# Kernel tuning notes

Measured on AMD Instinct MI355X. Metric: run time of the kernel, lower is better.

## Reference

```python
import jax, jax.numpy as jnp
import numpy as np

D_MODEL = 1024
NUM_HEADS = 16
D_K = D_MODEL // NUM_HEADS  # 64
THETA = 10000.0
B, S = 2, 2048


def _rope(x, cos, sin):
    # x: [b, h, s, d]; cos/sin: [s, d//2] (broadcast over b, h)
    x1 = x[..., 0::2]
    x2 = x[..., 1::2]
    y1 = x1 * cos - x2 * sin
    y2 = x1 * sin + x2 * cos
    # interleave back: stack on last dim then flatten pairs
    return jnp.stack([y1, y2], axis=-1).reshape(x.shape)


def setup_inputs() -> dict:
    key = jax.random.key(0)
    ks = jax.random.split(key, 5)
    scale = 1.0 / np.sqrt(D_MODEL)
    return {
        "x": jax.random.normal(ks[0], (B, S, D_MODEL), dtype=jnp.float32),
        "token_positions": jnp.arange(S, dtype=jnp.int32),
        "Wq": jax.random.normal(ks[1], (D_MODEL, D_MODEL), dtype=jnp.float32) * scale,
        "Wk": jax.random.normal(ks[2], (D_MODEL, D_MODEL), dtype=jnp.float32) * scale,
        "Wv": jax.random.normal(ks[3], (D_MODEL, D_MODEL), dtype=jnp.float32) * scale,
        "Wo": jax.random.normal(ks[4], (D_MODEL, D_MODEL), dtype=jnp.float32) * scale,
    }


def reference(x, token_positions, Wq, Wk, Wv, Wo):
    b, s, _ = x.shape
    # torch nn.Linear semantics (no bias in this repo's Linear): y = x @ W.T
    q = jnp.einsum("bsd,od->bso", x, Wq)
    k = jnp.einsum("bsd,od->bso", x, Wk)
    v = jnp.einsum("bsd,od->bso", x, Wv)
    # split heads: b s (h d) -> b h s d
    def split(t):
        return t.reshape(b, s, NUM_HEADS, D_K).transpose(0, 2, 1, 3)
    q, k, v = split(q), split(k), split(v)

    # RoPE tables
    inv_freq = 1.0 / (THETA ** (jnp.arange(0, D_K, 2, dtype=jnp.float32) / D_K))  # [d/2]
    freqs = token_positions.astype(jnp.float32)[:, None] * inv_freq[None, :]      # [s, d/2]
    cos, sin = jnp.cos(freqs), jnp.sin(freqs)
    q = _rope(q, cos, sin)
    k = _rope(k, cos, sin)

    scale = D_K ** (-0.5)
    scores = jnp.einsum("bhqd,bhkd->bhqk", q, k) * scale  # [b,h,s,s]
    causal = jnp.tril(jnp.ones((s, s), dtype=bool))
    scores = jnp.where(causal, scores, -jnp.inf)
    attn = jax.nn.softmax(scores, axis=-1)
    out = jnp.einsum("bhqk,bhkd->bhqd", attn, v)
    out = out.transpose(0, 2, 1, 3).reshape(b, s, D_MODEL)  # b h s d -> b s (h d)
    return jnp.einsum("bsd,od->bso", out, Wo)
```

## Files before the change

kernel.cpp:

```cpp
#include <hip/hip_runtime.h>
#include <hip/hip_bf16.h>
#include <math.h>

#define SS 2048

typedef __attribute__((ext_vector_type(8))) __bf16 bf16x8;
typedef __attribute__((ext_vector_type(4))) float f32x4;
typedef __attribute__((ext_vector_type(16))) float f32x16;
typedef __attribute__((ext_vector_type(4))) unsigned int u32x4;
typedef __attribute__((ext_vector_type(4))) unsigned short u16x4;

__device__ __forceinline__ f32x4 mfma16(bf16x8 a, bf16x8 b, f32x4 c) {
  return __builtin_amdgcn_mfma_f32_16x16x32_bf16(a, b, c, 0, 0, 0);
}
__device__ __forceinline__ f32x16 mfma32(bf16x8 a, bf16x8 b, f32x16 c) {
  return __builtin_amdgcn_mfma_f32_32x32x16_bf16(a, b, c, 0, 0, 0);
}

__device__ __forceinline__ void gld_lds16(const void* g, void* l) {
  __builtin_amdgcn_global_load_lds(
      (__attribute__((address_space(1))) void*)(g),
      (__attribute__((address_space(3))) void*)(l), 16, 0, 0);
}

#if __has_builtin(__builtin_amdgcn_exp2f)
#define EXP2F(x) __builtin_amdgcn_exp2f(x)
#else
#define EXP2F(x) __expf(0.69314718056f * (x))
#endif

__device__ __forceinline__ unsigned int cvtpk_bf16(float lo, float hi) {
  unsigned int r;
  asm("v_cvt_pk_bf16_f32 %0, %1, %2" : "=v"(r) : "v"(lo), "v"(hi));
  return r;
}
__device__ __forceinline__ void swap32(unsigned int& x, unsigned int& y) {
  asm("v_permlane32_swap_b32 %0, %1" : "+v"(x), "+v"(y));
}
__device__ __forceinline__ unsigned short bfu(float v) {
  __bf16 h = (__bf16)v;
  return __builtin_bit_cast(unsigned short, h);
}

__global__ void prep_kernel(const float* __restrict__ x, const float* __restrict__ Wq,
                            const float* __restrict__ Wk, const float* __restrict__ Wv,
                            const float* __restrict__ Wo, const int* __restrict__ pos,
                            __bf16* __restrict__ xb, __bf16* __restrict__ Wb,
                            float2* __restrict__ tab) {
  const int bid = blockIdx.x, tid = threadIdx.x;
  if (bid >= 4096) {
    int i = (bid - 4096) * 256 + tid;
    int s = i >> 5, j = i & 31;
    float p = (float)pos[s];
    float inv = exp2f((float)j * -0.41524101186098283f);
    float f = p * inv;
    float sn, cs;
    sincosf(f, &sn, &cs);
    tab[i] = make_float2(cs, sn);
    return;
  }
  const float* s;
  __bf16* d;
  size_t base;
  if (bid < 2048) { s = x; d = xb; base = bid; }
  else {
    int seg = (bid - 2048) >> 9;
    s = (seg == 0) ? Wq : (seg == 1) ? Wk : (seg == 2) ? Wv : Wo;
    d = Wb + (size_t)seg * 1024 * 1024;
    base = (bid - 2048) & 511;
  }
  size_t i = (base * 256 + tid) * 8;
  float4 a = *reinterpret_cast<const float4*>(s + i);
  float4 b = *reinterpret_cast<const float4*>(s + i + 4);
  bf16x8 o;
  o[0] = (__bf16)a.x; o[1] = (__bf16)a.y; o[2] = (__bf16)a.z; o[3] = (__bf16)a.w;
  o[4] = (__bf16)b.x; o[5] = (__bf16)b.y; o[6] = (__bf16)b.z; o[7] = (__bf16)b.w;
  *reinterpret_cast<bf16x8*>(d + i) = o;
}

__global__ __launch_bounds__(512, 1) void gemm256_kernel(
    const __bf16* __restrict__ A, const __bf16* __restrict__ Bw,
    __bf16* __restrict__ C, __bf16* __restrict__ Vt,
    const float2* __restrict__ tab) {
  const int K = 1024, N = 3072, nk = 32;
  __shared__ __align__(16) __bf16 sm[57344];
  __bf16* lsA = sm;
  __bf16* lsB = sm + 32768;

  const int tid = threadIdx.x;
  const int lane = tid & 63;
  const int wave = tid >> 6;
  const int wr = wave >> 2, wc = wave & 3;
  const bool lowW = wave < 6;

  const int xcd = blockIdx.x & 7;
  const int ii = blockIdx.x >> 3;
  const int m0 = (2 * xcd + (ii & 1)) * 256;
  const int n0 = (ii >> 1) * 192;

  const f32x4 fzero = {0.f, 0.f, 0.f, 0.f};
  f32x4 acc[8][3];
#pragma unroll
  for (int f = 0; f < 8; ++f)
#pragma unroll
    for (int g = 0; g < 3; ++g) acc[f][g] = fzero;

  const int arow0 = tid >> 2, ac = tid & 3;
  const __bf16* gA0 = A + (size_t)(m0 + arow0) * K + 8 * (ac ^ ((arow0 >> 1) & 3));
  const __bf16* gA1 = A + (size_t)(m0 + 128 + arow0) * K + 8 * (ac ^ (((arow0 + 128) >> 1) & 3));
  const int bid0 = tid, bid1 = tid + 384;
  const int br0 = bid0 >> 2, br1 = bid1 >> 2;
  const __bf16* gB0 = Bw + (size_t)(n0 + br0) * K + 8 * ((bid0 & 3) ^ ((br0 >> 1) & 3));
  const __bf16* gB1 = Bw + (size_t)(n0 + br1) * K + 8 * ((bid1 & 3) ^ ((br1 >> 1) & 3));

#define STAGE256(kt_)                                                \
  do {                                                               \
    const int kc_ = (kt_) & 3;                                       \
    const int ko_ = (kt_) * 32;                                      \
    gld_lds16(gA0 + ko_, lsA + kc_ * 8192 + tid * 8);                \
    gld_lds16(gA1 + ko_, lsA + kc_ * 8192 + 4096 + tid * 8);         \
    if (lowW) {                                                      \
      gld_lds16(gB0 + ko_, lsB + kc_ * 6144 + tid * 8);              \
      gld_lds16(gB1 + ko_, lsB + kc_ * 6144 + 3072 + tid * 8);       \
    }                                                                \
  } while (0)

  STAGE256(0);
  STAGE256(1);

  const int lrow = lane & 15, hi = lane >> 4;

#pragma unroll 1
  for (int kt = 0; kt < nk; ++kt) {
    const int ksA = (kt & 3) * 8192, ksB = (kt & 3) * 6144;
    if (kt + 2 < nk) {
      STAGE256(kt + 2);
      if (lowW) asm volatile("s_waitcnt vmcnt(8)" ::: "memory");
      else      asm volatile("s_waitcnt vmcnt(4)" ::: "memory");
    } else if (kt == nk - 2) {
      if (lowW) asm volatile("s_waitcnt vmcnt(4)" ::: "memory");
      else      asm volatile("s_waitcnt vmcnt(2)" ::: "memory");
    } else {
      asm volatile("s_waitcnt vmcnt(0)" ::: "memory");
    }
    __builtin_amdgcn_s_barrier();

    bf16x8 bfr[3];
#pragma unroll
    for (int g = 0; g < 3; ++g) {
      const int r = wc * 48 + g * 16 + lrow;
      bfr[g] = *reinterpret_cast<const bf16x8*>(
          lsB + ksB + r * 32 + ((hi ^ ((r >> 1) & 3)) * 8));
    }
    bf16x8 af[4];
#pragma unroll
    for (int f = 0; f < 4; ++f) {
      const int r = wr * 128 + f * 16 + lrow;
      af[f] = *reinterpret_cast<const bf16x8*>(
          lsA + ksA + r * 32 + ((hi ^ ((r >> 1) & 3)) * 8));
    }
    __builtin_amdgcn_s_setprio(1);
#pragma unroll
    for (int f = 0; f < 4; ++f)
#pragma unroll
      for (int g = 0; g < 3; ++g) acc[f][g] = mfma16(af[f], bfr[g], acc[f][g]);
    __builtin_amdgcn_s_setprio(0);
#pragma unroll
    for (int f = 0; f < 4; ++f) {
      const int r = wr * 128 + (f + 4) * 16 + lrow;
      af[f] = *reinterpret_cast<const bf16x8*>(
          lsA + ksA + r * 32 + ((hi ^ ((r >> 1) & 3)) * 8));
    }
    __builtin_amdgcn_s_setprio(1);
#pragma unroll
    for (int f = 0; f < 4; ++f)
#pragma unroll
      for (int g = 0; g < 3; ++g) acc[f + 4][g] = mfma16(af[f], bfr[g], acc[f + 4][g]);
    __builtin_amdgcn_s_setprio(0);
  }
#undef STAGE256

  const int crow = (lane >> 4) * 4, ccol = lane & 15;
  const int par = ccol & 1;
#pragma unroll
  for (int g = 0; g < 3; ++g) {
    const int cb = n0 + wc * 48 + g * 16;
    if (cb < 2048) {
      const int jj = ((cb + ccol) >> 1) & 31;
#pragma unroll
      for (int f = 0; f < 8; ++f) {
#pragma unroll
        for (int t = 0; t < 4; ++t) {
          const int r = m0 + wr * 128 + f * 16 + crow + t;
          const int s = r & (SS - 1);
          float2 cs = tab[(s << 5) | jj];
          float v = acc[f][g][t];
          float o = __shfl_xor(v, 1);
          float y = par ? fmaf(o, cs.y, v * cs.x) : fmaf(v, cs.x, -o * cs.y);
          C[(size_t)r * N + cb + ccol] = (__bf16)y;
        }
      }
    } else {
      const int c = cb - 2048 + ccol;
      const int hh = c >> 6, dd = c & 63;
#pragma unroll
      for (int f = 0; f < 8; ++f) {
        const int r0 = m0 + wr * 128 + f * 16 + crow;
        const int bb = r0 >> 11, s0 = r0 & (SS - 1);
        u16x4 pk;
#pragma unroll
        for (int t = 0; t < 4; ++t) pk[t] = bfu(acc[f][g][t]);
        *reinterpret_cast<u16x4*>(Vt + ((size_t)(bb * 16 + hh) * 64 + dd) * SS + s0) = pk;
      }
    }
  }
}

__global__ __launch_bounds__(512, 1) void gemm_out_kernel(
    const __bf16* __restrict__ A, const __bf16* __restrict__ Bw,
    float* __restrict__ C) {
  const int K = 1024, N = 1024, nk = 32;
  __shared__ __align__(16) __bf16 sm[32768];
  __bf16* lsA = sm;
  __bf16* lsB = sm + 16384;

  const int tid = threadIdx.x;
  const int lane = tid & 63;
  const int wave = tid >> 6;
  const int wr = wave >> 2, wc = wave & 3;

  const int xcd = blockIdx.x & 7;
  const int ii = blockIdx.x >> 3;
  const int m0 = (4 * xcd + (ii & 3)) * 128;
  const int n0 = (ii >> 2) * 128;

  const f32x4 fzero = {0.f, 0.f, 0.f, 0.f};
  f32x4 acc[4][2];
#pragma unroll
  for (int f = 0; f < 4; ++f)
#pragma unroll
    for (int g = 0; g < 2; ++g) acc[f][g] = fzero;

  const int srow = tid >> 2, sc = tid & 3;
  const int ssc = 8 * (sc ^ ((srow >> 1) & 3));
  const __bf16* gA = A + (size_t)(m0 + srow) * K + ssc;
  const __bf16* gB = Bw + (size_t)(n0 + srow) * K + ssc;

#define STAGEO(kt_)                                        \
  do {                                                     \
    const int kc_ = (kt_) & 3;                             \
    gld_lds16(gA + (kt_) * 32, lsA + kc_ * 4096 + tid * 8);\
    gld_lds16(gB + (kt_) * 32, lsB + kc_ * 4096 + tid * 8);\
  } while (0)

  STAGEO(0);
  STAGEO(1);

  const int lrow = lane & 15, hi = lane >> 4;

#pragma unroll 1
  for (int kt = 0; kt < nk; ++kt) {
    const int ks = (kt & 3) * 4096;
    if (kt + 2 < nk) {
      STAGEO(kt + 2);
      asm volatile("s_waitcnt vmcnt(4)" ::: "memory");
    } else if (kt == nk - 2) {
      asm volatile("s_waitcnt vmcnt(2)" ::: "memory");
    } else {
      asm volatile("s_waitcnt vmcnt(0)" ::: "memory");
    }
    __builtin_amdgcn_s_barrier();

    bf16x8 bfr[2], af[4];
#pragma unroll
    for (int g = 0; g < 2; ++g) {
      const int r = wc * 32 + g * 16 + lrow;
      bfr[g] = *reinterpret_cast<const bf16x8*>(
          lsB + ks + r * 32 + ((hi ^ ((r >> 1) & 3)) * 8));
    }
#pragma unroll
    for (int f = 0; f < 4; ++f) {
      const int r = wr * 64 + f * 16 + lrow;
      af[f] = *reinterpret_cast<const bf16x8*>(
          lsA + ks + r * 32 + ((hi ^ ((r >> 1) & 3)) * 8));
    }
    __builtin_amdgcn_s_setprio(1);
#pragma unroll
    for (int f = 0; f < 4; ++f)
#pragma unroll
      for (int g = 0; g < 2; ++g) acc[f][g] = mfma16(af[f], bfr[g], acc[f][g]);
    __builtin_amdgcn_s_setprio(0);
  }
#undef STAGEO

  const int crow = (lane >> 4) * 4, ccol = lane & 15;
#pragma unroll
  for (int f = 0; f < 4; ++f) {
#pragma unroll
    for (int g = 0; g < 2; ++g) {
      int r = m0 + wr * 64 + f * 16 + crow;
      int c = n0 + wc * 32 + g * 16 + ccol;
#pragma unroll
      for (int t = 0; t < 4; ++t) C[(size_t)(r + t) * N + c] = acc[f][g][t];
    }
  }
}

#define CEXP 0.18033688011112042f
#define SHIFT_B 16.0f

#define EXPSUM(S0, S1, L)                                                   \
  {                                                                         \
    float a0_ = 0.f, a1_ = 0.f, a2_ = 0.f, a3_ = 0.f;                       \
    _Pragma("unroll") for (int r = 0; r < 16; r += 4) {                     \
      S0[r] = EXP2F(fmaf(S0[r], CEXP, -SHIFT_B)); a0_ += S0[r];             \
      S0[r + 1] = EXP2F(fmaf(S0[r + 1], CEXP, -SHIFT_B)); a1_ += S0[r + 1]; \
      S0[r + 2] = EXP2F(fmaf(S0[r + 2], CEXP, -SHIFT_B)); a2_ += S0[r + 2]; \
      S0[r + 3] = EXP2F(fmaf(S0[r + 3], CEXP, -SHIFT_B)); a3_ += S0[r + 3]; \
    }                                                                       \
    _Pragma("unroll") for (int r = 0; r < 16; r += 4) {                     \
      S1[r] = EXP2F(fmaf(S1[r], CEXP, -SHIFT_B)); a0_ += S1[r];             \
      S1[r + 1] = EXP2F(fmaf(S1[r + 1], CEXP, -SHIFT_B)); a1_ += S1[r + 1]; \
      S1[r + 2] = EXP2F(fmaf(S1[r + 2], CEXP, -SHIFT_B)); a2_ += S1[r + 2]; \
      S1[r + 3] = EXP2F(fmaf(S1[r + 3], CEXP, -SHIFT_B)); a3_ += S1[r + 3]; \
    }                                                                       \
    float rs_ = (a0_ + a1_) + (a2_ + a3_);                                  \
    rs_ += __shfl_xor(rs_, 32);                                             \
    L += rs_;                                                               \
  }

template <int SPLIT>
__global__ __launch_bounds__(128) void attn_kernel(const __bf16* __restrict__ qkv,
                                                   const __bf16* __restrict__ Vt,
                                                   __bf16* __restrict__ pA,
                                                   __bf16* __restrict__ pB,
                                                   float* __restrict__ pL) {
  const int bid = blockIdx.x;
  const int x = bid & 7, t8 = bid >> 3;
  const int low = t8 & 7, phi = (t8 >> 3) & 3, g = (t8 >> 5) & 3;
  const int half = SPLIT ? (t8 >> 7) : 0;
  const int hp = phi * 8 + x;
  const int b = hp >> 4, h = hp & 15;
  const int qt = (g == 0) ? low : (g == 1) ? 31 - low : (g == 2) ? 15 - low : 16 + low;

  const int nkt = qt + 1;
  const int mid = (nkt + 1) >> 1;
  const int k0 = SPLIT ? (half ? mid : 0) : 0;
  const int k1 = SPLIT ? (half ? nkt : mid) : nkt;

  const int tid = threadIdx.x;
  const int wave = tid >> 6, lane = tid & 63;
  const int q32 = lane & 31, hi = lane >> 5;
  const int qw0 = qt * 64 + wave * 32;
  const int q = qw0 + q32;

  __shared__ __align__(16) __bf16 smem[16384];

  bf16x8 qb[4];
  {
    const __bf16* qr = qkv + (size_t)(b * SS + q) * 3072 + h * 64;
#pragma unroll
    for (int slot = 0; slot < 4; ++slot)
      qb[slot] = *reinterpret_cast<const bf16x8*>(qr + slot * 16 + hi * 8);
  }
  asm volatile("s_waitcnt vmcnt(0)" ::: "memory");

  const __bf16* kbase = qkv + (size_t)(b * SS) * 3072 + 1024 + h * 64;
  const __bf16* vbase = Vt + (size_t)((b * 16 + h) * 64) * SS;

  const int srow = tid >> 3, scg = tid & 7;
  const int ssc = 8 * (scg ^ (srow & 7));
  const __bf16* kG0 = kbase + (size_t)srow * 3072 + ssc;
  const __bf16* vG0 = vbase + (size_t)srow * SS + ssc;

#define STAGE(buf_, kt_)                                                      \
  do {                                                                        \
    const __bf16* kG = kG0 + (size_t)(kt_)*64 * 3072;                         \
    const __bf16* vG = vG0 + (size_t)(kt_)*64;                                \
    __bf16* sl_ = smem + (buf_)*8192;                                         \
    _Pragma("unroll") for (int u = 0; u < 4; ++u) {                           \
      gld_lds16(kG + (size_t)u * 16 * 3072, sl_ + tid * 8 + u * 1024);        \
      gld_lds16(vG + (size_t)u * 16 * SS, sl_ + 4096 + tid * 8 + u * 1024);   \
    }                                                                         \
  } while (0)

  const f32x16 fz16 = {0,0,0,0,0,0,0,0,0,0,0,0,0,0,0,0};
  f32x16 o0 = fz16, o1 = fz16;
  float lsum = 0.f;

  if (k0 < k1) STAGE(0, k0);

#pragma unroll 1
  for (int kt = k0; kt < k1; ++kt) {
    const int buf = (kt - k0) & 1;
    if (kt + 1 < k1) {
      STAGE(buf ^ 1, kt + 1);
      asm volatile("s_waitcnt vmcnt(8)" ::: "memory");
    } else {
      asm volatile("s_waitcnt vmcnt(0)" ::: "memory");
    }
    __builtin_amdgcn_s_barrier();

    const __bf16* lk = smem + buf * 8192;
    const __bf16* lv = lk + 4096;

    f32x16 s0 = fz16, s1 = fz16;
    __builtin_amdgcn_s_setprio(1);
#pragma unroll
    for (int slot = 0; slot < 4; ++slot) {
      const int swz = 8 * ((slot * 2 + hi) ^ (q32 & 7));
      bf16x8 kf0 = *reinterpret_cast<const bf16x8*>(lk + q32 * 64 + swz);
      bf16x8 kf1 = *reinterpret_cast<const bf16x8*>(lk + (32 + q32) * 64 + swz);
      s0 = mfma32(kf0, qb[slot], s0);
      s1 = mfma32(kf1, qb[slot], s1);
    }
    __builtin_amdgcn_s_setprio(0);

    if (kt == qt) {
      const int kvb = kt * 64;
#pragma unroll
      for (int r = 0; r < 16; ++r) {
        const int rowc = (r & 3) + 8 * (r >> 2) + 4 * hi;
        if (kvb + rowc > q) s0[r] = -INFINITY;
        if (kvb + 32 + rowc > q) s1[r] = -INFINITY;
      }
    }

    EXPSUM(s0, s1, lsum)

    bf16x8 pb[4];
    {
      unsigned int A = cvtpk_bf16(s0[0], s0[1]), B2 = cvtpk_bf16(s0[2], s0[3]);
      unsigned int C2 = cvtpk_bf16(s0[4], s0[5]), D2 = cvtpk_bf16(s0[6], s0[7]);
      swap32(A, C2); swap32(B2, D2);
      u32x4 t0 = {A, B2, C2, D2};
      pb[0] = __builtin_bit_cast(bf16x8, t0);
      unsigned int E = cvtpk_bf16(s0[8], s0[9]), F = cvtpk_bf16(s0[10], s0[11]);
      unsigned int G = cvtpk_bf16(s0[12], s0[13]), H = cvtpk_bf16(s0[14], s0[15]);
      swap32(E, G); swap32(F, H);
      u32x4 t1 = {E, F, G, H};
      pb[1] = __builtin_bit_cast(bf16x8, t1);
      unsigned int A3 = cvtpk_bf16(s1[0], s1[1]), B3 = cvtpk_bf16(s1[2], s1[3]);
      unsigned int C3 = cvtpk_bf16(s1[4], s1[5]), D3 = cvtpk_bf16(s1[6], s1[7]);
      swap32(A3, C3); swap32(B3, D3);
      u32x4 t2 = {A3, B3, C3, D3};
      pb[2] = __builtin_bit_cast(bf16x8, t2);
      unsigned int E3 = cvtpk_bf16(s1[8], s1[9]), F3 = cvtpk_bf16(s1[10], s1[11]);
      unsigned int G3 = cvtpk_bf16(s1[12], s1[13]), H3 = cvtpk_bf16(s1[14], s1[15]);
      swap32(E3, G3); swap32(F3, H3);
      u32x4 t3 = {E3, F3, G3, H3};
      pb[3] = __builtin_bit_cast(bf16x8, t3);
    }

    __builtin_amdgcn_s_setprio(1);
#pragma unroll
    for (int slot = 0; slot < 4; ++slot) {
      const int swz = 8 * ((slot * 2 + hi) ^ (q32 & 7));
      bf16x8 v0 = *reinterpret_cast<const bf16x8*>(lv + q32 * 64 + swz);
      bf16x8 v1 = *reinterpret_cast<const bf16x8*>(lv + (32 + q32) * 64 + swz);
      o0 = mfma32(v0, pb[slot], o0);
      o1 = mfma32(v1, pb[slot], o1);
    }
    __builtin_amdgcn_s_setprio(0);

    __builtin_amdgcn_s_barrier();
  }

  asm volatile("s_waitcnt vmcnt(0)" ::: "memory");
  __builtin_amdgcn_s_barrier();

  const float inv = SPLIT ? 1.0f : (1.0f / lsum);
  __bf16* ol = smem + wave * 2304;
#pragma unroll
  for (int r = 0; r < 16; ++r) {
    const int d = (r & 3) + 8 * (r >> 2) + 4 * hi;
    if (SPLIT) {
      ol[q32 * 72 + d] = (__bf16)o0[r];
      ol[q32 * 72 + 32 + d] = (__bf16)o1[r];
    } else {
      ol[q32 * 72 + d] = (__bf16)(o0[r] * inv);
      ol[q32 * 72 + 32 + d] = (__bf16)(o1[r] * inv);
    }
  }
  __bf16* dst = (SPLIT && half) ? pB : pA;
#pragma unroll
  for (int pass = 0; pass < 4; ++pass) {
    const int idx = pass * 64 + lane;
    const int row = idx >> 3, colc = idx & 7;
    bf16x8 v = *reinterpret_cast<const bf16x8*>(ol + row * 72 + colc * 8);
    *reinterpret_cast<bf16x8*>(
        dst + (size_t)(b * SS + qt * 64 + wave * 32 + row) * 1024 + h * 64 + colc * 8) = v;
  }
  if (SPLIT && hi == 0)
    pL[half * 65536 + hp * 2048 + qt * 64 + wave * 32 + q32] = lsum;
}

__global__ void combine_kernel(const __bf16* __restrict__ pB,
                               const float* __restrict__ pL,
                               __bf16* __restrict__ ao) {
  const int i = (blockIdx.x * 256 + threadIdx.x) * 8;
  const int row = i >> 10, col = i & 1023;
  const int bb = row >> 11, s = row & 2047, h = col >> 6;
  const int bh = bb * 16 + h;
  const float lA = pL[bh * 2048 + s];
  const float lB = pL[65536 + bh * 2048 + s];
  const float inv = 1.0f / (lA + lB);
  bf16x8 a = *reinterpret_cast<const bf16x8*>(ao + i);
  bf16x8 b8 = *reinterpret_cast<const bf16x8*>(pB + i);
  bf16x8 o;
#pragma unroll
  for (int j = 0; j < 8; ++j) o[j] = (__bf16)(((float)a[j] + (float)b8[j]) * inv);
  *reinterpret_cast<bf16x8*>(ao + i) = o;
}

extern "C" void kernel_launch(void* const* d_in, const int* in_sizes, int n_in,
                              void* d_out, int out_size, void* d_ws, size_t ws_size,
                              hipStream_t stream) {
  const float* x  = (const float*)d_in[0];
  const int* pos  = (const int*)d_in[1];
  const float* Wq = (const float*)d_in[2];
  const float* Wk = (const float*)d_in[3];
  const float* Wv = (const float*)d_in[4];
  const float* Wo = (const float*)d_in[5];

  __bf16* xb  = (__bf16*)d_ws;
  __bf16* Wb  = xb + (size_t)4096 * 1024;
  __bf16* qkv = Wb + (size_t)4096 * 1024;
  __bf16* Vt  = qkv + (size_t)4096 * 3072;
  __bf16* ao  = Vt + (size_t)2048 * 2048;
  float2* tab = (float2*)(ao + (size_t)4096 * 1024);
  __bf16* pB  = (__bf16*)(tab + 2048 * 32);
  float*  pL  = (float*)(pB + (size_t)4096 * 1024);

  const size_t NEED = (size_t)(pL + 2 * 32 * 2048) - (size_t)d_ws;

  prep_kernel<<<4352, 256, 0, stream>>>(x, Wq, Wk, Wv, Wo, pos, xb, Wb, tab);
  gemm256_kernel<<<256, 512, 0, stream>>>(xb, Wb, qkv, Vt, tab);
  if (ws_size >= NEED) {
    attn_kernel<1><<<2048, 128, 0, stream>>>(qkv, Vt, ao, pB, pL);
    combine_kernel<<<2048, 256, 0, stream>>>(pB, pL, ao);
  } else {
    attn_kernel<0><<<1024, 128, 0, stream>>>(qkv, Vt, ao, nullptr, nullptr);
  }
  gemm_out_kernel<<<256, 512, 0, stream>>>(ao, Wb + (size_t)3 * 1024 * 1024, (float*)d_out);
}
```

Baseline: 113.0 us.

## Pair short and long causal query tiles per block for balanced attention work

Replaces the split-KV attention kernel with a paired scheme: each block processes query tile pi and its complement 31-pi, so every block runs 16 or 17 KV rounds. Only the long tiles (second half of the sequence) are split across two blocks, so the combine kernel now touches half the rows and the grid shrinks to 1024 blocks. The aim is balanced per-block work with less partial-output traffic and combine work. It drops the small-workspace fallback and keeps two Q fragments and two accumulator sets live, raising register pressure.

```diff
diff --git a/kernel.cpp b/kernel.cpp
--- a/kernel.cpp
+++ b/kernel.cpp
@@ -309,59 +309,118 @@
 #define CEXP 0.18033688011112042f
 #define SHIFT_B 16.0f
 
-#define EXPSUM(S0, S1, L)                                                   \
-  {                                                                         \
-    float a0_ = 0.f, a1_ = 0.f, a2_ = 0.f, a3_ = 0.f;                       \
-    _Pragma("unroll") for (int r = 0; r < 16; r += 4) {                     \
-      S0[r] = EXP2F(fmaf(S0[r], CEXP, -SHIFT_B)); a0_ += S0[r];             \
-      S0[r + 1] = EXP2F(fmaf(S0[r + 1], CEXP, -SHIFT_B)); a1_ += S0[r + 1]; \
-      S0[r + 2] = EXP2F(fmaf(S0[r + 2], CEXP, -SHIFT_B)); a2_ += S0[r + 2]; \
-      S0[r + 3] = EXP2F(fmaf(S0[r + 3], CEXP, -SHIFT_B)); a3_ += S0[r + 3]; \
-    }                                                                       \
-    _Pragma("unroll") for (int r = 0; r < 16; r += 4) {                     \
-      S1[r] = EXP2F(fmaf(S1[r], CEXP, -SHIFT_B)); a0_ += S1[r];             \
-      S1[r + 1] = EXP2F(fmaf(S1[r + 1], CEXP, -SHIFT_B)); a1_ += S1[r + 1]; \
-      S1[r + 2] = EXP2F(fmaf(S1[r + 2], CEXP, -SHIFT_B)); a2_ += S1[r + 2]; \
-      S1[r + 3] = EXP2F(fmaf(S1[r + 3], CEXP, -SHIFT_B)); a3_ += S1[r + 3]; \
-    }                                                                       \
-    float rs_ = (a0_ + a1_) + (a2_ + a3_);                                  \
-    rs_ += __shfl_xor(rs_, 32);                                             \
-    L += rs_;                                                               \
-  }
-
-template <int SPLIT>
-__global__ __launch_bounds__(128) void attn_kernel(const __bf16* __restrict__ qkv,
-                                                   const __bf16* __restrict__ Vt,
-                                                   __bf16* __restrict__ pA,
-                                                   __bf16* __restrict__ pB,
-                                                   float* __restrict__ pL) {
+__device__ __forceinline__ void attn_round(const __bf16* lk, const __bf16* lv,
+                                           const bf16x8 (&qb)[4], f32x16& o0,
+                                           f32x16& o1, float& lsum, int q,
+                                           int kvb, bool diag, int q32, int hi) {
+  const f32x16 fz16 = {0,0,0,0,0,0,0,0,0,0,0,0,0,0,0,0};
+  f32x16 s0 = fz16, s1 = fz16;
+  __builtin_amdgcn_s_setprio(1);
+#pragma unroll
+  for (int slot = 0; slot < 4; ++slot) {
+    const int swz = 8 * ((slot * 2 + hi) ^ (q32 & 7));
+    bf16x8 kf0 = *reinterpret_cast<const bf16x8*>(lk + q32 * 64 + swz);
+    bf16x8 kf1 = *reinterpret_cast<const bf16x8*>(lk + (32 + q32) * 64 + swz);
+    s0 = mfma32(kf0, qb[slot], s0);
+    s1 = mfma32(kf1, qb[slot], s1);
+  }
+  __builtin_amdgcn_s_setprio(0);
+
+  if (diag) {
+#pragma unroll
+    for (int r = 0; r < 16; ++r) {
+      const int rowc = (r & 3) + 8 * (r >> 2) + 4 * hi;
+      if (kvb + rowc > q) s0[r] = -INFINITY;
+      if (kvb + 32 + rowc > q) s1[r] = -INFINITY;
+    }
+  }
+
+  {
+    float a0 = 0.f, a1 = 0.f, a2 = 0.f, a3 = 0.f;
+#pragma unroll
+    for (int r = 0; r < 16; r += 4) {
+      s0[r] = EXP2F(fmaf(s0[r], CEXP, -SHIFT_B)); a0 += s0[r];
+      s0[r + 1] = EXP2F(fmaf(s0[r + 1], CEXP, -SHIFT_B)); a1 += s0[r + 1];
+      s0[r + 2] = EXP2F(fmaf(s0[r + 2], CEXP, -SHIFT_B)); a2 += s0[r + 2];
+      s0[r + 3] = EXP2F(fmaf(s0[r + 3], CEXP, -SHIFT_B)); a3 += s0[r + 3];
+    }
+#pragma unroll
+    for (int r = 0; r < 16; r += 4) {
+      s1[r] = EXP2F(fmaf(s1[r], CEXP, -SHIFT_B)); a0 += s1[r];
+      s1[r + 1] = EXP2F(fmaf(s1[r + 1], CEXP, -SHIFT_B)); a1 += s1[r + 1];
+      s1[r + 2] = EXP2F(fmaf(s1[r + 2], CEXP, -SHIFT_B)); a2 += s1[r + 2];
+      s1[r + 3] = EXP2F(fmaf(s1[r + 3], CEXP, -SHIFT_B)); a3 += s1[r + 3];
+    }
+    float rs = (a0 + a1) + (a2 + a3);
+    rs += __shfl_xor(rs, 32);
+    lsum += rs;
+  }
+
+  bf16x8 pb[4];
+  {
+    unsigned int A = cvtpk_bf16(s0[0], s0[1]), B2 = cvtpk_bf16(s0[2], s0[3]);
+    unsigned int C2 = cvtpk_bf16(s0[4], s0[5]), D2 = cvtpk_bf16(s0[6], s0[7]);
+    swap32(A, C2); swap32(B2, D2);
+    u32x4 t0 = {A, B2, C2, D2};
+    pb[0] = __builtin_bit_cast(bf16x8, t0);
+    unsigned int E = cvtpk_bf16(s0[8], s0[9]), F = cvtpk_bf16(s0[10], s0[11]);
+    unsigned int G = cvtpk_bf16(s0[12], s0[13]), H = cvtpk_bf16(s0[14], s0[15]);
+    swap32(E, G); swap32(F, H);
+    u32x4 t1 = {E, F, G, H};
+    pb[1] = __builtin_bit_cast(bf16x8, t1);
+    unsigned int A3 = cvtpk_bf16(s1[0], s1[1]), B3 = cvtpk_bf16(s1[2], s1[3]);
+    unsigned int C3 = cvtpk_bf16(s1[4], s1[5]), D3 = cvtpk_bf16(s1[6], s1[7]);
+    swap32(A3, C3); swap32(B3, D3);
+    u32x4 t2 = {A3, B3, C3, D3};
+    pb[2] = __builtin_bit_cast(bf16x8, t2);
+    unsigned int E3 = cvtpk_bf16(s1[8], s1[9]), F3 = cvtpk_bf16(s1[10], s1[11]);
+    unsigned int G3 = cvtpk_bf16(s1[12], s1[13]), H3 = cvtpk_bf16(s1[14], s1[15]);
+    swap32(E3, G3); swap32(F3, H3);
+    u32x4 t3 = {E3, F3, G3, H3};
+    pb[3] = __builtin_bit_cast(bf16x8, t3);
+  }
+
+  __builtin_amdgcn_s_setprio(1);
+#pragma unroll
+  for (int slot = 0; slot < 4; ++slot) {
+    const int swz = 8 * ((slot * 2 + hi) ^ (q32 & 7));
+    bf16x8 v0 = *reinterpret_cast<const bf16x8*>(lv + q32 * 64 + swz);
+    bf16x8 v1 = *reinterpret_cast<const bf16x8*>(lv + (32 + q32) * 64 + swz);
+    o0 = mfma32(v0, pb[slot], o0);
+    o1 = mfma32(v1, pb[slot], o1);
+  }
+  __builtin_amdgcn_s_setprio(0);
+}
+
+__global__ __launch_bounds__(128) void attn_pair_kernel(
+    const __bf16* __restrict__ qkv, const __bf16* __restrict__ Vt,
+    __bf16* __restrict__ AO, __bf16* __restrict__ pB, float* __restrict__ pL) {
   const int bid = blockIdx.x;
-  const int x = bid & 7, t8 = bid >> 3;
-  const int low = t8 & 7, phi = (t8 >> 3) & 3, g = (t8 >> 5) & 3;
-  const int half = SPLIT ? (t8 >> 7) : 0;
+  const int x = bid & 7, t7 = bid >> 3;
+  const int phi = t7 & 3, pi = (t7 >> 2) & 15, half = t7 >> 6;
   const int hp = phi * 8 + x;
   const int b = hp >> 4, h = hp & 15;
-  const int qt = (g == 0) ? low : (g == 1) ? 31 - low : (g == 2) ? 15 - low : 16 + low;
-
-  const int nkt = qt + 1;
-  const int mid = (nkt + 1) >> 1;
-  const int k0 = SPLIT ? (half ? mid : 0) : 0;
-  const int k1 = SPLIT ? (half ? nkt : mid) : nkt;
+  const int qtA = pi, qtB = 31 - pi;
+  const int nr = half ? 16 : 17;
+  const int segA = half ? 0 : (pi + 1);
 
   const int tid = threadIdx.x;
   const int wave = tid >> 6, lane = tid & 63;
   const int q32 = lane & 31, hi = lane >> 5;
-  const int qw0 = qt * 64 + wave * 32;
-  const int q = qw0 + q32;
+  const int qA = qtA * 64 + wave * 32 + q32;
+  const int qB = qtB * 64 + wave * 32 + q32;
 
   __shared__ __align__(16) __bf16 smem[16384];
 
-  bf16x8 qb[4];
+  bf16x8 qbA[4], qbB[4];
   {
-    const __bf16* qr = qkv + (size_t)(b * SS + q) * 3072 + h * 64;
-#pragma unroll
-    for (int slot = 0; slot < 4; ++slot)
-      qb[slot] = *reinterpret_cast<const bf16x8*>(qr + slot * 16 + hi * 8);
+    const __bf16* qrA = qkv + (size_t)(b * SS + qA) * 3072 + h * 64;
+    const __bf16* qrB = qkv + (size_t)(b * SS + qB) * 3072 + h * 64;
+#pragma unroll
+    for (int slot = 0; slot < 4; ++slot) {
+      qbA[slot] = *reinterpret_cast<const bf16x8*>(qrA + slot * 16 + hi * 8);
+      qbB[slot] = *reinterpret_cast<const bf16x8*>(qrB + slot * 16 + hi * 8);
+    }
   }
   asm volatile("s_waitcnt vmcnt(0)" ::: "memory");
 
@@ -373,10 +432,12 @@
   const __bf16* kG0 = kbase + (size_t)srow * 3072 + ssc;
   const __bf16* vG0 = vbase + (size_t)srow * SS + ssc;
 
-#define STAGE(buf_, kt_)                                                      \
+#define KVOF(r_) (half ? (16 - pi + (r_)) : (((r_) < segA) ? (r_) : ((r_)-segA)))
+
+#define STAGE(buf_, kv_)                                                      \
   do {                                                                        \
-    const __bf16* kG = kG0 + (size_t)(kt_)*64 * 3072;                         \
-    const __bf16* vG = vG0 + (size_t)(kt_)*64;                                \
+    const __bf16* kG = kG0 + (size_t)(kv_)*64 * 3072;                         \
+    const __bf16* vG = vG0 + (size_t)(kv_)*64;                                \
     __bf16* sl_ = smem + (buf_)*8192;                                         \
     _Pragma("unroll") for (int u = 0; u < 4; ++u) {                           \
       gld_lds16(kG + (size_t)u * 16 * 3072, sl_ + tid * 8 + u * 1024);        \
@@ -385,16 +446,16 @@
   } while (0)
 
   const f32x16 fz16 = {0,0,0,0,0,0,0,0,0,0,0,0,0,0,0,0};
-  f32x16 o0 = fz16, o1 = fz16;
-  float lsum = 0.f;
-
-  if (k0 < k1) STAGE(0, k0);
+  f32x16 oA0 = fz16, oA1 = fz16, oB0 = fz16, oB1 = fz16;
+  float lA = 0.f, lB = 0.f;
+
+  STAGE(0, KVOF(0));
 
 #pragma unroll 1
-  for (int kt = k0; kt < k1; ++kt) {
-    const int buf = (kt - k0) & 1;
-    if (kt + 1 < k1) {
-      STAGE(buf ^ 1, kt + 1);
+  for (int r = 0; r < nr; ++r) {
+    const int buf = r & 1;
+    if (r + 1 < nr) {
+      STAGE(buf ^ 1, KVOF(r + 1));
       asm volatile("s_waitcnt vmcnt(8)" ::: "memory");
     } else {
       asm volatile("s_waitcnt vmcnt(0)" ::: "memory");
@@ -403,108 +464,85 @@
 
     const __bf16* lk = smem + buf * 8192;
     const __bf16* lv = lk + 4096;
-
-    f32x16 s0 = fz16, s1 = fz16;
-    __builtin_amdgcn_s_setprio(1);
-#pragma unroll
-    for (int slot = 0; slot < 4; ++slot) {
-      const int swz = 8 * ((slot * 2 + hi) ^ (q32 & 7));
-      bf16x8 kf0 = *reinterpret_cast<const bf16x8*>(lk + q32 * 64 + swz);
-      bf16x8 kf1 = *reinterpret_cast<const bf16x8*>(lk + (32 + q32) * 64 + swz);
-      s0 = mfma32(kf0, qb[slot], s0);
-      s1 = mfma32(kf1, qb[slot], s1);
-    }
-    __builtin_amdgcn_s_setprio(0);
-
-    if (kt == qt) {
-      const int kvb = kt * 64;
-#pragma unroll
-      for (int r = 0; r < 16; ++r) {
-        const int rowc = (r & 3) + 8 * (r >> 2) + 4 * hi;
-        if (kvb + rowc > q) s0[r] = -INFINITY;
-        if (kvb + 32 + rowc > q) s1[r] = -INFINITY;
-      }
-    }
-
-    EXPSUM(s0, s1, lsum)
-
-    bf16x8 pb[4];
-    {
-      unsigned int A = cvtpk_bf16(s0[0], s0[1]), B2 = cvtpk_bf16(s0[2], s0[3]);
-      unsigned int C2 = cvtpk_bf16(s0[4], s0[5]), D2 = cvtpk_bf16(s0[6], s0[7]);
-      swap32(A, C2); swap32(B2, D2);
-      u32x4 t0 = {A, B2, C2, D2};
-      pb[0] = __builtin_bit_cast(bf16x8, t0);
-      unsigned int E = cvtpk_bf16(s0[8], s0[9]), F = cvtpk_bf16(s0[10], s0[11]);
-      unsigned int G = cvtpk_bf16(s0[12], s0[13]), H = cvtpk_bf16(s0[14], s0[15]);
-      swap32(E, G); swap32(F, H);
-      u32x4 t1 = {E, F, G, H};
-      pb[1] = __builtin_bit_cast(bf16x8, t1);
-      unsigned int A3 = cvtpk_bf16(s1[0], s1[1]), B3 = cvtpk_bf16(s1[2], s1[3]);
-      unsigned int C3 = cvtpk_bf16(s1[4], s1[5]), D3 = cvtpk_bf16(s1[6], s1[7]);
-      swap32(A3, C3); swap32(B3, D3);
-      u32x4 t2 = {A3, B3, C3, D3};
-      pb[2] = __builtin_bit_cast(bf16x8, t2);
-      unsigned int E3 = cvtpk_bf16(s1[8], s1[9]), F3 = cvtpk_bf16(s1[10], s1[11]);
-      unsigned int G3 = cvtpk_bf16(s1[12], s1[13]), H3 = cvtpk_bf16(s1[14], s1[15]);
-      swap32(E3, G3); swap32(F3, H3);
-      u32x4 t3 = {E3, F3, G3, H3};
-      pb[3] = __builtin_bit_cast(bf16x8, t3);
-    }
-
-    __builtin_amdgcn_s_setprio(1);
-#pragma unroll
-    for (int slot = 0; slot < 4; ++slot) {
-      const int swz = 8 * ((slot * 2 + hi) ^ (q32 & 7));
-      bf16x8 v0 = *reinterpret_cast<const bf16x8*>(lv + q32 * 64 + swz);
-      bf16x8 v1 = *reinterpret_cast<const bf16x8*>(lv + (32 + q32) * 64 + swz);
-      o0 = mfma32(v0, pb[slot], o0);
-      o1 = mfma32(v1, pb[slot], o1);
-    }
-    __builtin_amdgcn_s_setprio(0);
+    const int kv = KVOF(r);
+
+    if (r < segA) {
+      attn_round(lk, lv, qbA, oA0, oA1, lA, qA, kv * 64, kv == qtA, q32, hi);
+    } else {
+      attn_round(lk, lv, qbB, oB0, oB1, lB, qB, kv * 64, kv == qtB, q32, hi);
+    }
 
     __builtin_amdgcn_s_barrier();
   }
+#undef STAGE
+#undef KVOF
 
   asm volatile("s_waitcnt vmcnt(0)" ::: "memory");
   __builtin_amdgcn_s_barrier();
 
-  const float inv = SPLIT ? 1.0f : (1.0f / lsum);
   __bf16* ol = smem + wave * 2304;
-#pragma unroll
-  for (int r = 0; r < 16; ++r) {
-    const int d = (r & 3) + 8 * (r >> 2) + 4 * hi;
-    if (SPLIT) {
-      ol[q32 * 72 + d] = (__bf16)o0[r];
-      ol[q32 * 72 + 32 + d] = (__bf16)o1[r];
-    } else {
-      ol[q32 * 72 + d] = (__bf16)(o0[r] * inv);
-      ol[q32 * 72 + 32 + d] = (__bf16)(o1[r] * inv);
-    }
-  }
-  __bf16* dst = (SPLIT && half) ? pB : pA;
-#pragma unroll
-  for (int pass = 0; pass < 4; ++pass) {
-    const int idx = pass * 64 + lane;
-    const int row = idx >> 3, colc = idx & 7;
-    bf16x8 v = *reinterpret_cast<const bf16x8*>(ol + row * 72 + colc * 8);
-    *reinterpret_cast<bf16x8*>(
-        dst + (size_t)(b * SS + qt * 64 + wave * 32 + row) * 1024 + h * 64 + colc * 8) = v;
-  }
-  if (SPLIT && hi == 0)
-    pL[half * 65536 + hp * 2048 + qt * 64 + wave * 32 + q32] = lsum;
+  if (half == 0) {
+    const float invA = 1.0f / lA;
+#pragma unroll
+    for (int r = 0; r < 16; ++r) {
+      const int d = (r & 3) + 8 * (r >> 2) + 4 * hi;
+      ol[q32 * 72 + d] = (__bf16)(oA0[r] * invA);
+      ol[q32 * 72 + 32 + d] = (__bf16)(oA1[r] * invA);
+    }
+#pragma unroll
+    for (int pass = 0; pass < 4; ++pass) {
+      const int idx = pass * 64 + lane;
+      const int row = idx >> 3, colc = idx & 7;
+      bf16x8 v = *reinterpret_cast<const bf16x8*>(ol + row * 72 + colc * 8);
+      *reinterpret_cast<bf16x8*>(
+          AO + (size_t)(b * SS + qtA * 64 + wave * 32 + row) * 1024 + h * 64 + colc * 8) = v;
+    }
+#pragma unroll
+    for (int r = 0; r < 16; ++r) {
+      const int d = (r & 3) + 8 * (r >> 2) + 4 * hi;
+      ol[q32 * 72 + d] = (__bf16)oB0[r];
+      ol[q32 * 72 + 32 + d] = (__bf16)oB1[r];
+    }
+#pragma unroll
+    for (int pass = 0; pass < 4; ++pass) {
+      const int idx = pass * 64 + lane;
+      const int row = idx >> 3, colc = idx & 7;
+      bf16x8 v = *reinterpret_cast<const bf16x8*>(ol + row * 72 + colc * 8);
+      *reinterpret_cast<bf16x8*>(
+          AO + (size_t)(b * SS + qtB * 64 + wave * 32 + row) * 1024 + h * 64 + colc * 8) = v;
+    }
+    if (hi == 0) pL[hp * 2048 + qtB * 64 + wave * 32 + q32] = lB;
+  } else {
+#pragma unroll
+    for (int r = 0; r < 16; ++r) {
+      const int d = (r & 3) + 8 * (r >> 2) + 4 * hi;
+      ol[q32 * 72 + d] = (__bf16)oB0[r];
+      ol[q32 * 72 + 32 + d] = (__bf16)oB1[r];
+    }
+#pragma unroll
+    for (int pass = 0; pass < 4; ++pass) {
+      const int idx = pass * 64 + lane;
+      const int row = idx >> 3, colc = idx & 7;
+      bf16x8 v = *reinterpret_cast<const bf16x8*>(ol + row * 72 + colc * 8);
+      *reinterpret_cast<bf16x8*>(
+          pB + (size_t)(b * SS + qtB * 64 + wave * 32 + row) * 1024 + h * 64 + colc * 8) = v;
+    }
+    if (hi == 0) pL[65536 + hp * 2048 + qtB * 64 + wave * 32 + q32] = lB;
+  }
 }
 
 __global__ void combine_kernel(const __bf16* __restrict__ pB,
                                const float* __restrict__ pL,
                                __bf16* __restrict__ ao) {
-  const int i = (blockIdx.x * 256 + threadIdx.x) * 8;
-  const int row = i >> 10, col = i & 1023;
-  const int bb = row >> 11, s = row & 2047, h = col >> 6;
+  const int e = (blockIdx.x * 256 + threadIdx.x) * 8;
+  const int subrow = e >> 10, col = e & 1023;
+  const int bb = subrow >> 10, s = 1024 + (subrow & 1023);
+  const int h = col >> 6;
   const int bh = bb * 16 + h;
-  const float lA = pL[bh * 2048 + s];
-  const float lB = pL[65536 + bh * 2048 + s];
-  const float inv = 1.0f / (lA + lB);
+  const size_t i = ((size_t)bb * SS + s) * 1024 + col;
+  const float la = pL[bh * 2048 + s];
+  const float lb = pL[65536 + bh * 2048 + s];
+  const float inv = 1.0f / (la + lb);
   bf16x8 a = *reinterpret_cast<const bf16x8*>(ao + i);
   bf16x8 b8 = *reinterpret_cast<const bf16x8*>(pB + i);
   bf16x8 o;
@@ -532,15 +570,9 @@
   __bf16* pB  = (__bf16*)(tab + 2048 * 32);
   float*  pL  = (float*)(pB + (size_t)4096 * 1024);
 
-  const size_t NEED = (size_t)(pL + 2 * 32 * 2048) - (size_t)d_ws;
-
   prep_kernel<<<4352, 256, 0, stream>>>(x, Wq, Wk, Wv, Wo, pos, xb, Wb, tab);
   gemm256_kernel<<<256, 512, 0, stream>>>(xb, Wb, qkv, Vt, tab);
-  if (ws_size >= NEED) {
-    attn_kernel<1><<<2048, 128, 0, stream>>>(qkv, Vt, ao, pB, pL);
-    combine_kernel<<<2048, 256, 0, stream>>>(pB, pL, ao);
-  } else {
-    attn_kernel<0><<<1024, 128, 0, stream>>>(qkv, Vt, ao, nullptr, nullptr);
-  }
+  attn_pair_kernel<<<1024, 128, 0, stream>>>(qkv, Vt, ao, pB, pL);
+  combine_kernel<<<1024, 256, 0, stream>>>(pB, pL, ao);
   gemm_out_kernel<<<256, 512, 0, stream>>>(ao, Wb + (size_t)3 * 1024 * 1024, (float*)d_out);
 }
```

After: 100.3 us, median of 2. -11.2%, faster.
